# Performance work log

Hardware: AMD Instinct MI355X
Metric: run time of the kernel (lower is better)

## Reference

```python
import jax, jax.numpy as jnp
import numpy as np

B, D_IN, T = 8, 1024, 2048
CODEBOOK_SIZE, CODEBOOK_DIM = 8192, 8
EPS = 1e-12  # F.normalize default eps


def _l2_normalize(x, axis=-1):
    # matches torch F.normalize: x / max(||x||_2, eps)
    n = jnp.sqrt(jnp.sum(x * x, axis=axis, keepdims=True))
    return x / jnp.maximum(n, EPS)


def setup_inputs() -> dict:
    key = jax.random.key(0)
    k_z, k_wi, k_bi, k_wo, k_bo, k_cb = jax.random.split(key, 6)
    z = jax.random.normal(k_z, (B, D_IN, T), dtype=jnp.float32)
    # weight_norm(Conv1d) is a reparameterization; the effective weight is a
    # plain [out, in] matrix for a kernel_size=1 conv.
    w_in = jax.random.normal(k_wi, (CODEBOOK_DIM, D_IN), dtype=jnp.float32) * (1.0 / np.sqrt(D_IN))
    b_in = jax.random.normal(k_bi, (CODEBOOK_DIM,), dtype=jnp.float32) * 0.01
    w_out = jax.random.normal(k_wo, (D_IN, CODEBOOK_DIM), dtype=jnp.float32) * (1.0 / np.sqrt(CODEBOOK_DIM))
    b_out = jax.random.normal(k_bo, (D_IN,), dtype=jnp.float32) * 0.01
    codebook = jax.random.normal(k_cb, (CODEBOOK_SIZE, CODEBOOK_DIM), dtype=jnp.float32)
    return {"z": z, "w_in": w_in, "b_in": b_in, "w_out": w_out, "b_out": b_out, "codebook": codebook}


def reference(z, w_in, b_in, w_out, b_out, codebook):
    b, _, t = z.shape
    # in_project: 1x1 conv == matmul over channel dim
    z_e = jnp.einsum('od,bdt->bot', w_in, z) + b_in[None, :, None]  # [B, cd, T]

    # decode_latents
    enc = z_e.transpose(0, 2, 1).reshape(b * t, CODEBOOK_DIM)  # (b t) d
    enc_n = _l2_normalize(enc, axis=1)
    cb_n = _l2_normalize(codebook, axis=1)
    # dist = ||e||^2 - 2 e @ c^T + ||c||^2  (materializes [B*T, K] as original)
    dist = (jnp.sum(enc_n * enc_n, axis=1, keepdims=True)
            - 2.0 * (enc_n @ cb_n.T)
            + jnp.sum(cb_n * cb_n, axis=1)[None, :])
    indices = jnp.argmax(-dist, axis=1).reshape(b, t)  # [B, T] int
    # decode_code uses the UNnormalized codebook
    z_q = codebook[indices].transpose(0, 2, 1)  # [B, cd, T]

    # straight-through estimator
    z_q_st = z_e + jax.lax.stop_gradient(z_q - z_e)
    out = jnp.einsum('od,bdt->bot', w_out, z_q_st) + b_out[None, :, None]  # [B, D, T]

    commit_loss = jnp.zeros((b,), dtype=z.dtype)
    codebook_loss = jnp.zeros((b,), dtype=z.dtype)
    return (out, commit_loss, codebook_loss, indices, z_e)
```

## Files before the change

### kernel.cpp

```cpp
#include <hip/hip_runtime.h>
#include <math.h>

static constexpr int Bq  = 8;
static constexpr int DIN = 1024;
static constexpr int TTT = 2048;
static constexpr int KCB = 8192;

static constexpr int NCH = 64;
static constexpr int CPC = 128;

static constexpr size_t OUT_OFS  = 0;
static constexpr size_t LOSS_OFS = (size_t)Bq * DIN * TTT;
static constexpr size_t IDX_OFS  = LOSS_OFS + 16;
static constexpr size_t ZE_OFS   = IDX_OFS + (size_t)Bq * TTT;

static constexpr size_t WS_CBN  = 0;
static constexpr size_t WS_C2   = 65536;
static constexpr size_t WS_WT   = 73728;
static constexpr size_t WS_ENC  = 81920;
static constexpr size_t WS_PART = 212992;
static constexpr size_t WS_IDXI = WS_PART + (size_t)NCH * 16384;

__device__ __forceinline__ void load_enc_neg_norm(const float* __restrict__ ws,
                                                  int r, float4& ma, float4& mb) {
  const float4* ep = (const float4*)(ws + WS_ENC + (size_t)r * 8);
  float4 a = ep[0], c = ep[1];
  float n2 = 0.f;
  n2 = fmaf(a.x, a.x, n2); n2 = fmaf(a.y, a.y, n2);
  n2 = fmaf(a.z, a.z, n2); n2 = fmaf(a.w, a.w, n2);
  n2 = fmaf(c.x, c.x, n2); n2 = fmaf(c.y, c.y, n2);
  n2 = fmaf(c.z, c.z, n2); n2 = fmaf(c.w, c.w, n2);
  float dn = fmaxf(sqrtf(n2), 1e-12f);
  ma.x = -(a.x / dn); ma.y = -(a.y / dn);
  ma.z = -(a.z / dn); ma.w = -(a.w / dn);
  mb.x = -(c.x / dn); mb.y = -(c.y / dn);
  mb.z = -(c.z / dn); mb.w = -(c.w / dn);
}

__device__ __forceinline__ float score8(const float4& ma, const float4& mb,
                                        const float4& c0, const float4& c1, float cc) {
  float s = fmaf(ma.x, c0.x, cc);
  s = fmaf(ma.y, c0.y, s); s = fmaf(ma.z, c0.z, s); s = fmaf(ma.w, c0.w, s);
  s = fmaf(mb.x, c1.x, s); s = fmaf(mb.y, c1.y, s);
  s = fmaf(mb.z, c1.z, s); s = fmaf(mb.w, c1.w, s);
  return s;
}

__global__ __launch_bounds__(256) void k0_prep(
    const float* __restrict__ w_in, const float* __restrict__ codebook,
    float* __restrict__ ws, float* __restrict__ out)
{
  int tid = blockIdx.x * 256 + threadIdx.x;
  if (tid < KCB) {
    const float4* cp = (const float4*)(codebook + (size_t)tid * 8);
    float4 a = cp[0], b = cp[1];
    float v[8] = {a.x, a.y, a.z, a.w, b.x, b.y, b.z, b.w};
    float n2 = 0.f;
#pragma unroll
    for (int o = 0; o < 8; o++) n2 = fmaf(v[o], v[o], n2);
    float dn = fmaxf(sqrtf(n2), 1e-12f);
    float u[8];
    float s2 = 0.f;
#pragma unroll
    for (int o = 0; o < 8; o++) { u[o] = v[o] / dn; s2 = fmaf(u[o], u[o], s2); }
    float4* wp = (float4*)(ws + WS_CBN + (size_t)tid * 8);
    wp[0] = make_float4(u[0], u[1], u[2], u[3]);
    wp[1] = make_float4(u[4], u[5], u[6], u[7]);
    ws[WS_C2 + tid] = 0.5f * s2;
  } else if (tid < KCB + DIN) {
    int d = tid - KCB;
#pragma unroll
    for (int o = 0; o < 8; o++) ws[WS_WT + (size_t)d * 8 + o] = w_in[(size_t)o * DIN + d];
  } else if (tid < KCB + DIN + 16) {
    out[LOSS_OFS + (tid - KCB - DIN)] = 0.f;
  }
}

__global__ __launch_bounds__(512) void k1_proj_in(
    const float* __restrict__ z, const float* __restrict__ b_in,
    float* __restrict__ ws, float* __restrict__ out)
{
  __shared__ __align__(16) float lds[16384];
  int tid = threadIdx.x;
  int bx = blockIdx.x;
  int b = bx >> 5;
  int t0 = (bx & 31) << 6;
  {
    const float4* src = (const float4*)(ws + WS_WT);
    float4* dst = (float4*)lds;
#pragma unroll
    for (int i = 0; i < 4; i++) dst[tid + 512 * i] = src[tid + 512 * i];
  }
  __syncthreads();
  int tt = tid & 15;
  int dg = tid >> 4;
  const float* zb = z + (size_t)b * DIN * TTT + t0 + (tt << 2);
  float4 acc[8];
#pragma unroll
  for (int o = 0; o < 8; o++) acc[o] = make_float4(0.f, 0.f, 0.f, 0.f);
  int dbase = dg << 5;
  const float4* wl = (const float4*)lds;
#pragma unroll 8
  for (int i = 0; i < 32; i++) {
    int d = dbase + i;
    float4 zv = *(const float4*)(zb + (size_t)d * TTT);
    float4 w0 = wl[d * 2 + 0];
    float4 w1 = wl[d * 2 + 1];
#define ACC1(o, wsc)                                    \
    acc[o].x = fmaf(wsc, zv.x, acc[o].x);               \
    acc[o].y = fmaf(wsc, zv.y, acc[o].y);               \
    acc[o].z = fmaf(wsc, zv.z, acc[o].z);               \
    acc[o].w = fmaf(wsc, zv.w, acc[o].w);
    ACC1(0, w0.x) ACC1(1, w0.y) ACC1(2, w0.z) ACC1(3, w0.w)
    ACC1(4, w1.x) ACC1(5, w1.y) ACC1(6, w1.z) ACC1(7, w1.w)
#undef ACC1
  }
  __syncthreads();
  {
    float4* pl = (float4*)lds;
#pragma unroll
    for (int o = 0; o < 8; o++) pl[dg * 128 + o * 16 + tt] = acc[o];
  }
  __syncthreads();
  int o = tid >> 6;
  int t = tid & 63;
  float s = 0.f;
#pragma unroll
  for (int g = 0; g < 32; g++) s += lds[g * 512 + o * 64 + t];
  s += b_in[o];
  out[ZE_OFS + ((size_t)b * 8 + o) * TTT + t0 + t] = s;
  ws[WS_ENC + ((size_t)(b * TTT + t0 + t)) * 8 + o] = s;
}

__global__ __launch_bounds__(256) void k2_scan(float* __restrict__ ws)
{
  __shared__ __align__(16) float4 scb[CPC * 2];
  __shared__ float sch[CPC];
  int tid = threadIdx.x;
  int rb = blockIdx.x >> 6;
  int ch = blockIdx.x & 63;
  int k0 = ch << 7;
  if (tid < CPC) {
    const float4* src = (const float4*)(ws + WS_CBN + (size_t)(k0 + tid) * 8);
    scb[tid * 2]     = src[0];
    scb[tid * 2 + 1] = src[1];
    sch[tid] = ws[WS_C2 + k0 + tid];
  }
  int rbase = (rb << 10) + tid;

  float4 m0a, m0b, m1a, m1b, m2a, m2b, m3a, m3b;
  load_enc_neg_norm(ws, rbase,       m0a, m0b);
  load_enc_neg_norm(ws, rbase + 256, m1a, m1b);
  load_enc_neg_norm(ws, rbase + 512, m2a, m2b);
  load_enc_neg_norm(ws, rbase + 768, m3a, m3b);
  float b0 = 3.4e38f, b1 = 3.4e38f, b2 = 3.4e38f, b3 = 3.4e38f;

  __syncthreads();
#pragma unroll 2
  for (int k = 0; k < CPC; k += 2) {
    float4 c00 = scb[2 * k + 0];
    float4 c01 = scb[2 * k + 1];
    float4 c10 = scb[2 * k + 2];
    float4 c11 = scb[2 * k + 3];
    float ca = sch[k];
    float cb = sch[k + 1];
#define STEP2(ma, mb, bj) {                                                   \
    float s0 = score8(ma, mb, c00, c01, ca);                                  \
    float s1 = score8(ma, mb, c10, c11, cb);                                  \
    asm("v_min3_f32 %0, %1, %2, %3" : "=v"(bj) : "v"(bj), "v"(s0), "v"(s1)); }
    STEP2(m0a, m0b, b0)
    STEP2(m1a, m1b, b1)
    STEP2(m2a, m2b, b2)
    STEP2(m3a, m3b, b3)
#undef STEP2
  }
  float* part = ws + WS_PART + (size_t)ch * 16384 + rbase;
  part[0]   = b0;
  part[256] = b1;
  part[512] = b2;
  part[768] = b3;
}

__global__ __launch_bounds__(256) void k2b_argmin(float* __restrict__ ws, float* __restrict__ out)
{
  int gtid = blockIdx.x * 256 + threadIdx.x;
  int r = gtid >> 2;
  int sub = gtid & 3;
  const float* part = ws + WS_PART;
  float m = 3.4e38f;
  int cbest = NCH;
  int ch0 = sub << 4;
#pragma unroll 4
  for (int i = 0; i < 16; i++) {
    int ch = ch0 + i;
    float p = part[(size_t)ch * 16384 + r];
    if (p < m) { m = p; cbest = ch; }
  }
#pragma unroll
  for (int off = 1; off <= 2; off <<= 1) {
    float om = __shfl_xor(m, off);
    int oc = __shfl_xor(cbest, off);
    if (om < m || (om == m && oc < cbest)) { m = om; cbest = oc; }
  }
  float4 ma, mb;
  load_enc_neg_norm(ws, r, ma, mb);
  int base = (cbest << 7) + (sub << 5);
  float best = 3.4e38f;
  int bi = 0x7fffffff;
#pragma unroll 4
  for (int k = 0; k < 32; k++) {
    const float4* cp = (const float4*)(ws + WS_CBN + (size_t)(base + k) * 8);
    float4 c0 = cp[0], c1 = cp[1];
    float cc = ws[WS_C2 + base + k];
    float s = score8(ma, mb, c0, c1, cc);
    if (s < best) { best = s; bi = base + k; }
  }
#pragma unroll
  for (int off = 1; off <= 2; off <<= 1) {
    float os = __shfl_xor(best, off);
    int oi = __shfl_xor(bi, off);
    if (os < best || (os == best && oi < bi)) { best = os; bi = oi; }
  }
  if (sub == 0) {
    out[IDX_OFS + r] = (float)bi;
    ((int*)(ws + WS_IDXI))[r] = bi;
  }
}

__global__ __launch_bounds__(256) void k3_proj_out(
    const float* __restrict__ codebook, const float* __restrict__ w_out,
    const float* __restrict__ b_out, const float* __restrict__ ws,
    float* __restrict__ out)
{
  int bx = blockIdx.x;
  int b = bx >> 7;
  int th = (bx >> 6) & 1;
  int dt = bx & 63;
  int tid = threadIdx.x;
  int t = (th << 10) + (tid << 2);
  const int* idxp = (const int*)(ws + WS_IDXI);
  int4 id = *(const int4*)(idxp + b * TTT + t);
  const float4* cbp = (const float4*)codebook;
  float4 c00 = cbp[(size_t)id.x * 2], c01 = cbp[(size_t)id.x * 2 + 1];
  float4 c10 = cbp[(size_t)id.y * 2], c11 = cbp[(size_t)id.y * 2 + 1];
  float4 c20 = cbp[(size_t)id.z * 2], c21 = cbp[(size_t)id.z * 2 + 1];
  float4 c30 = cbp[(size_t)id.w * 2], c31 = cbp[(size_t)id.w * 2 + 1];
  int d0 = dt << 4;
#pragma unroll 4
  for (int dd = 0; dd < 16; dd++) {
    int d = d0 + dd;
    const float* wr = w_out + (size_t)d * 8;
    float w0 = wr[0], w1 = wr[1], w2 = wr[2], w3 = wr[3];
    float w4 = wr[4], w5 = wr[5], w6 = wr[6], w7 = wr[7];
    float bb = b_out[d];
#define DOT8(lo, hi)                                                          \
    fmaf(w7, hi.w, fmaf(w6, hi.z, fmaf(w5, hi.y, fmaf(w4, hi.x,              \
    fmaf(w3, lo.w, fmaf(w2, lo.z, fmaf(w1, lo.y, fmaf(w0, lo.x, bb))))))))
    float4 r;
    r.x = DOT8(c00, c01);
    r.y = DOT8(c10, c11);
    r.z = DOT8(c20, c21);
    r.w = DOT8(c30, c31);
#undef DOT8
    *(float4*)(out + OUT_OFS + ((size_t)b * DIN + d) * TTT + t) = r;
  }
}

extern "C" void kernel_launch(void* const* d_in, const int* in_sizes, int n_in,
                              void* d_out, int out_size, void* d_ws, size_t ws_size,
                              hipStream_t stream) {
  const float* z        = (const float*)d_in[0];
  const float* w_in     = (const float*)d_in[1];
  const float* b_in     = (const float*)d_in[2];
  const float* w_out    = (const float*)d_in[3];
  const float* b_out    = (const float*)d_in[4];
  const float* codebook = (const float*)d_in[5];
  float* out = (float*)d_out;
  float* ws  = (float*)d_ws;

  k0_prep<<<dim3(37), dim3(256), 0, stream>>>(w_in, codebook, ws, out);
  k1_proj_in<<<dim3(256), dim3(512), 0, stream>>>(z, b_in, ws, out);
  k2_scan<<<dim3(1024), dim3(256), 0, stream>>>(ws);
  k2b_argmin<<<dim3(256), dim3(256), 0, stream>>>(ws, out);
  k3_proj_out<<<dim3(1024), dim3(256), 0, stream>>>(codebook, w_out, b_out, ws, out);
}
```

Measured before the change: 183.6 us.

## Run codebook distance scan on bf16x3 MFMA with bounded exact-refinement argmin

Replaces the scalar FP32 distance scan with MFMA 32x32x16 bf16 matmuls that emulate higher precision by splitting operands into high and low bf16 parts (three products). The -0.5||c||^2 bias is folded in as an extra K column. The scan now takes a per-row max over 1024-entry chunks, 8 chunks in total. The argmin kernel then rescans, in exact FP32, only the chunks whose approximate minimum lies within an error bound of the best, and falls back to a full scan if none qualifies. This moves most of the work onto matrix cores. It relies on the assumed error bound E_BOUND and pays extra refinement work whenever several chunks are near-ties.

```diff
diff --git a/kernel.cpp b/kernel.cpp
--- a/kernel.cpp
+++ b/kernel.cpp
@@ -6,20 +6,35 @@
 static constexpr int TTT = 2048;
 static constexpr int KCB = 8192;
 
-static constexpr int NCH = 64;
-static constexpr int CPC = 128;
+static constexpr int NCHA = 8;
+static constexpr int CPCA = 1024;
+static constexpr float E_BOUND = 2.5e-4f;
 
 static constexpr size_t OUT_OFS  = 0;
 static constexpr size_t LOSS_OFS = (size_t)Bq * DIN * TTT;
 static constexpr size_t IDX_OFS  = LOSS_OFS + 16;
 static constexpr size_t ZE_OFS   = IDX_OFS + (size_t)Bq * TTT;
 
-static constexpr size_t WS_CBN  = 0;
-static constexpr size_t WS_C2   = 65536;
-static constexpr size_t WS_WT   = 73728;
-static constexpr size_t WS_ENC  = 81920;
-static constexpr size_t WS_PART = 212992;
-static constexpr size_t WS_IDXI = WS_PART + (size_t)NCH * 16384;
+static constexpr size_t WS_CBN   = 0;
+static constexpr size_t WS_C2    = 65536;
+static constexpr size_t WS_WT    = 73728;
+static constexpr size_t WS_ENC   = 81920;
+static constexpr size_t WS_FRAGH = 212992;
+static constexpr size_t WS_FRAGL = 278528;
+static constexpr size_t WS_PART  = 344064;
+static constexpr size_t WS_IDXI  = WS_PART + (size_t)NCHA * 16384;
+
+typedef __attribute__((ext_vector_type(8)))  short bf16x8;
+typedef __attribute__((ext_vector_type(16))) float f32x16;
+
+__device__ __forceinline__ unsigned short bf16_rn(float x) {
+  unsigned u = __float_as_uint(x);
+  unsigned r = (u + 0x7FFFu + ((u >> 16) & 1u)) >> 16;
+  return (unsigned short)r;
+}
+__device__ __forceinline__ float bf16_to_f(unsigned short h) {
+  return __uint_as_float(((unsigned)h) << 16);
+}
 
 __device__ __forceinline__ void load_enc_neg_norm(const float* __restrict__ ws,
                                                   int r, float4& ma, float4& mb) {
@@ -46,6 +61,19 @@
   return s;
 }
 
+__device__ __forceinline__ void scan_slice(const float* __restrict__ ws, int base,
+                                           const float4& ma, const float4& mb,
+                                           float& best, int& bi) {
+#pragma unroll 4
+  for (int k = 0; k < 128; k++) {
+    const float4* cp = (const float4*)(ws + WS_CBN + (size_t)(base + k) * 8);
+    float4 c0 = cp[0], c1 = cp[1];
+    float cc = ws[WS_C2 + base + k];
+    float s = score8(ma, mb, c0, c1, cc);
+    if (s < best) { best = s; bi = base + k; }
+  }
+}
+
 __global__ __launch_bounds__(256) void k0_prep(
     const float* __restrict__ w_in, const float* __restrict__ codebook,
     float* __restrict__ ws, float* __restrict__ out)
@@ -66,7 +94,36 @@
     float4* wp = (float4*)(ws + WS_CBN + (size_t)tid * 8);
     wp[0] = make_float4(u[0], u[1], u[2], u[3]);
     wp[1] = make_float4(u[4], u[5], u[6], u[7]);
-    ws[WS_C2 + tid] = 0.5f * s2;
+    float cc = 0.5f * s2;
+    ws[WS_C2 + tid] = cc;
+
+    unsigned short h[16], l[16];
+#pragma unroll
+    for (int o = 0; o < 16; o++) { h[o] = 0; l[o] = 0; }
+#pragma unroll
+    for (int o = 0; o < 8; o++) {
+      unsigned short hh = bf16_rn(u[o]);
+      h[o] = hh;
+      l[o] = bf16_rn(u[o] - bf16_to_f(hh));
+    }
+    {
+      unsigned short hh = bf16_rn(-cc);
+      h[8] = hh;
+      l[8] = bf16_rn(-cc - bf16_to_f(hh));
+    }
+    int cgrp = tid >> 10;
+    int tl   = (tid >> 5) & 31;
+    int lcol = tid & 31;
+    size_t fb = (size_t)cgrp * 16384 + (size_t)tl * 512;
+    unsigned short* FH = (unsigned short*)(ws + WS_FRAGH);
+    unsigned short* FL = (unsigned short*)(ws + WS_FRAGL);
+#pragma unroll
+    for (int e = 0; e < 8; e++) {
+      FH[fb + (size_t)lcol * 8 + e]        = h[e];
+      FH[fb + (size_t)(lcol + 32) * 8 + e] = h[8 + e];
+      FL[fb + (size_t)lcol * 8 + e]        = l[e];
+      FL[fb + (size_t)(lcol + 32) * 8 + e] = l[8 + e];
+    }
   } else if (tid < KCB + DIN) {
     int d = tid - KCB;
 #pragma unroll
@@ -134,96 +191,137 @@
 
 __global__ __launch_bounds__(256) void k2_scan(float* __restrict__ ws)
 {
-  __shared__ __align__(16) float4 scb[CPC * 2];
-  __shared__ float sch[CPC];
+  __shared__ __align__(16) unsigned short lh[16384];
+  __shared__ __align__(16) unsigned short ll[16384];
   int tid = threadIdx.x;
-  int rb = blockIdx.x >> 6;
-  int ch = blockIdx.x & 63;
-  int k0 = ch << 7;
-  if (tid < CPC) {
-    const float4* src = (const float4*)(ws + WS_CBN + (size_t)(k0 + tid) * 8);
-    scb[tid * 2]     = src[0];
-    scb[tid * 2 + 1] = src[1];
-    sch[tid] = ws[WS_C2 + k0 + tid];
-  }
-  int rbase = (rb << 10) + tid;
-
-  float4 m0a, m0b, m1a, m1b, m2a, m2b, m3a, m3b;
-  load_enc_neg_norm(ws, rbase,       m0a, m0b);
-  load_enc_neg_norm(ws, rbase + 256, m1a, m1b);
-  load_enc_neg_norm(ws, rbase + 512, m2a, m2b);
-  load_enc_neg_norm(ws, rbase + 768, m3a, m3b);
-  float b0 = 3.4e38f, b1 = 3.4e38f, b2 = 3.4e38f, b3 = 3.4e38f;
-
+  int rg = blockIdx.x >> 3;
+  int ch = blockIdx.x & 7;
+  {
+    const float4* srcH = (const float4*)(ws + WS_FRAGH) + (size_t)ch * 2048;
+    const float4* srcL = (const float4*)(ws + WS_FRAGL) + (size_t)ch * 2048;
+    float4* dH = (float4*)lh;
+    float4* dL = (float4*)ll;
+#pragma unroll
+    for (int i = 0; i < 8; i++) {
+      dH[tid + 256 * i] = srcH[tid + 256 * i];
+      dL[tid + 256 * i] = srcL[tid + 256 * i];
+    }
+  }
+  int lane = tid & 63;
+  int wv = tid >> 6;
+  int rowbase = rg * 128 + wv * 32;
+  int row = rowbase + (lane & 31);
+
+  bf16x8 eh, el;
+#pragma unroll
+  for (int o = 0; o < 8; o++) { eh[o] = 0; el[o] = 0; }
+  {
+    const float4* ep = (const float4*)(ws + WS_ENC + (size_t)row * 8);
+    float4 a = ep[0], c = ep[1];
+    float n2 = 0.f;
+    n2 = fmaf(a.x, a.x, n2); n2 = fmaf(a.y, a.y, n2);
+    n2 = fmaf(a.z, a.z, n2); n2 = fmaf(a.w, a.w, n2);
+    n2 = fmaf(c.x, c.x, n2); n2 = fmaf(c.y, c.y, n2);
+    n2 = fmaf(c.z, c.z, n2); n2 = fmaf(c.w, c.w, n2);
+    float dn = fmaxf(sqrtf(n2), 1e-12f);
+    float v[8] = {a.x / dn, a.y / dn, a.z / dn, a.w / dn,
+                  c.x / dn, c.y / dn, c.z / dn, c.w / dn};
+    if (lane < 32) {
+#pragma unroll
+      for (int o = 0; o < 8; o++) {
+        unsigned short hh = bf16_rn(v[o]);
+        eh[o] = (short)hh;
+        el[o] = (short)bf16_rn(v[o] - bf16_to_f(hh));
+      }
+    } else {
+      eh[0] = (short)0x3F80;
+    }
+  }
   __syncthreads();
-#pragma unroll 2
-  for (int k = 0; k < CPC; k += 2) {
-    float4 c00 = scb[2 * k + 0];
-    float4 c01 = scb[2 * k + 1];
-    float4 c10 = scb[2 * k + 2];
-    float4 c11 = scb[2 * k + 3];
-    float ca = sch[k];
-    float cb = sch[k + 1];
-#define STEP2(ma, mb, bj) {                                                   \
-    float s0 = score8(ma, mb, c00, c01, ca);                                  \
-    float s1 = score8(ma, mb, c10, c11, cb);                                  \
-    asm("v_min3_f32 %0, %1, %2, %3" : "=v"(bj) : "v"(bj), "v"(s0), "v"(s1)); }
-    STEP2(m0a, m0b, b0)
-    STEP2(m1a, m1b, b1)
-    STEP2(m2a, m2b, b2)
-    STEP2(m3a, m3b, b3)
-#undef STEP2
-  }
-  float* part = ws + WS_PART + (size_t)ch * 16384 + rbase;
-  part[0]   = b0;
-  part[256] = b1;
-  part[512] = b2;
-  part[768] = b3;
+
+  f32x16 rmax;
+#pragma unroll
+  for (int i = 0; i < 16; i++) rmax[i] = -3.4e38f;
+
+  for (int t2 = 0; t2 < 32; t2 += 2) {
+    bf16x8 bh0 = *(const bf16x8*)(&lh[((size_t)t2 * 64 + lane) * 8]);
+    bf16x8 bl0 = *(const bf16x8*)(&ll[((size_t)t2 * 64 + lane) * 8]);
+    bf16x8 bh1 = *(const bf16x8*)(&lh[((size_t)(t2 + 1) * 64 + lane) * 8]);
+    bf16x8 bl1 = *(const bf16x8*)(&ll[((size_t)(t2 + 1) * 64 + lane) * 8]);
+    f32x16 accA, accB;
+#pragma unroll
+    for (int i = 0; i < 16; i++) { accA[i] = 0.f; accB[i] = 0.f; }
+    accA = __builtin_amdgcn_mfma_f32_32x32x16_bf16(eh, bh0, accA, 0, 0, 0);
+    accA = __builtin_amdgcn_mfma_f32_32x32x16_bf16(eh, bl0, accA, 0, 0, 0);
+    accA = __builtin_amdgcn_mfma_f32_32x32x16_bf16(el, bh0, accA, 0, 0, 0);
+    accB = __builtin_amdgcn_mfma_f32_32x32x16_bf16(eh, bh1, accB, 0, 0, 0);
+    accB = __builtin_amdgcn_mfma_f32_32x32x16_bf16(eh, bl1, accB, 0, 0, 0);
+    accB = __builtin_amdgcn_mfma_f32_32x32x16_bf16(el, bh1, accB, 0, 0, 0);
+#pragma unroll
+    for (int i = 0; i < 16; i++) rmax[i] = fmaxf(fmaxf(rmax[i], accA[i]), accB[i]);
+  }
+
+#pragma unroll
+  for (int off = 1; off <= 16; off <<= 1) {
+#pragma unroll
+    for (int i = 0; i < 16; i++) rmax[i] = fmaxf(rmax[i], __shfl_xor(rmax[i], off));
+  }
+  if ((lane & 31) == 0) {
+    int rb2 = rowbase + 4 * (lane >> 5);
+#pragma unroll
+    for (int i = 0; i < 16; i++) {
+      int rr = (i & 3) + 8 * (i >> 2);
+      ws[WS_PART + (size_t)ch * 16384 + rb2 + rr] = -rmax[i];
+    }
+  }
 }
 
 __global__ __launch_bounds__(256) void k2b_argmin(float* __restrict__ ws, float* __restrict__ out)
 {
   int gtid = blockIdx.x * 256 + threadIdx.x;
-  int r = gtid >> 2;
-  int sub = gtid & 3;
-  const float* part = ws + WS_PART;
-  float m = 3.4e38f;
-  int cbest = NCH;
-  int ch0 = sub << 4;
-#pragma unroll 4
-  for (int i = 0; i < 16; i++) {
-    int ch = ch0 + i;
-    float p = part[(size_t)ch * 16384 + r];
-    if (p < m) { m = p; cbest = ch; }
-  }
-#pragma unroll
-  for (int off = 1; off <= 2; off <<= 1) {
-    float om = __shfl_xor(m, off);
-    int oc = __shfl_xor(cbest, off);
-    if (om < m || (om == m && oc < cbest)) { m = om; cbest = oc; }
-  }
+  int r = gtid >> 3;
+  int sub = gtid & 7;
+  int lane = threadIdx.x & 63;
+  float p = ws[WS_PART + (size_t)sub * 16384 + r];
+  float m = p;
+#pragma unroll
+  for (int off = 1; off <= 4; off <<= 1) m = fminf(m, __shfl_xor(m, off));
+  float thr = m + 2.0f * E_BOUND;
+
   float4 ma, mb;
   load_enc_neg_norm(ws, r, ma, mb);
-  int base = (cbest << 7) + (sub << 5);
+
   float best = 3.4e38f;
   int bi = 0x7fffffff;
-#pragma unroll 4
-  for (int k = 0; k < 32; k++) {
-    const float4* cp = (const float4*)(ws + WS_CBN + (size_t)(base + k) * 8);
-    float4 c0 = cp[0], c1 = cp[1];
-    float cc = ws[WS_C2 + base + k];
-    float s = score8(ma, mb, c0, c1, cc);
-    if (s < best) { best = s; bi = base + k; }
-  }
-#pragma unroll
-  for (int off = 1; off <= 2; off <<= 1) {
-    float os = __shfl_xor(best, off);
-    int oi = __shfl_xor(bi, off);
-    if (os < best || (os == best && oi < bi)) { best = os; bi = oi; }
+  for (int ch = 0; ch < NCHA; ch++) {
+    float pc = __shfl(p, (lane & 56) | ch);
+    if (pc <= thr) {
+      scan_slice(ws, (ch << 10) + (sub << 7), ma, mb, best, bi);
+    }
+  }
+  float rbest = best;
+  int rbi = bi;
+#pragma unroll
+  for (int off = 1; off <= 4; off <<= 1) {
+    float os = __shfl_xor(rbest, off);
+    int oi = __shfl_xor(rbi, off);
+    if (os < rbest || (os == rbest && oi < rbi)) { rbest = os; rbi = oi; }
+  }
+  if (rbest > thr) {
+    best = 3.4e38f; bi = 0x7fffffff;
+    for (int ch = 0; ch < NCHA; ch++)
+      scan_slice(ws, (ch << 10) + (sub << 7), ma, mb, best, bi);
+    rbest = best; rbi = bi;
+#pragma unroll
+    for (int off = 1; off <= 4; off <<= 1) {
+      float os = __shfl_xor(rbest, off);
+      int oi = __shfl_xor(rbi, off);
+      if (os < rbest || (os == rbest && oi < rbi)) { rbest = os; rbi = oi; }
+    }
   }
   if (sub == 0) {
-    out[IDX_OFS + r] = (float)bi;
-    ((int*)(ws + WS_IDXI))[r] = bi;
+    out[IDX_OFS + r] = (float)rbi;
+    ((int*)(ws + WS_IDXI))[r] = rbi;
   }
 }
 
@@ -281,6 +379,6 @@
   k0_prep<<<dim3(37), dim3(256), 0, stream>>>(w_in, codebook, ws, out);
   k1_proj_in<<<dim3(256), dim3(512), 0, stream>>>(z, b_in, ws, out);
   k2_scan<<<dim3(1024), dim3(256), 0, stream>>>(ws);
-  k2b_argmin<<<dim3(256), dim3(256), 0, stream>>>(ws, out);
+  k2b_argmin<<<dim3(512), dim3(256), 0, stream>>>(ws, out);
   k3_proj_out<<<dim3(1024), dim3(256), 0, stream>>>(codebook, w_out, b_out, ws, out);
 }
```

Measured after the change: 320.5 us. 1.75x slower.
